# Optimization experiments

Measured on AMD Instinct MI355X. Metric: run time of the kernel, lower is better.

## Reference

```python
import jax, jax.numpy as jnp
import numpy as np

H, D = 16, 64            # heads_num, mouse_hidden_dim // heads_num
START_FRAME = 9728       # current_start (token units)
GLOBAL_END_PREV = 9728   # kv_cache['global_end_index'] before this call
LOCAL_END_PREV = 9728    # kv_cache['local_end_index'] before this call
SINK = 0                 # sink_tokens in source
WINDOW = 8192            # max_attention_size = local_attn_size (token units)


def _rope_interleaved(x, cos_h, sin_h):
    # non-neox (interleaved) rotary: x [B,S,H,D], cos_h/sin_h [S, D//2]
    x1 = x[..., 0::2]
    x2 = x[..., 1::2]
    c = cos_h[None, :, None, :]
    s = sin_h[None, :, None, :]
    o1 = x1 * c - x2 * s
    o2 = x2 * c + x1 * s
    return jnp.stack([o1, o2], axis=-1).reshape(x.shape)


def setup_inputs() -> dict:
    key = jax.random.key(0)
    ks = jax.random.split(key, 7)
    B, S, C = 1, 1024, 10240
    return {
        'q': jax.random.normal(ks[0], (B, S, H, D), jnp.float32),
        'k': jax.random.normal(ks[1], (B, S, H, D), jnp.float32),
        'v': jax.random.normal(ks[2], (B, S, H, D), jnp.float32),
        'cache_k': jax.random.normal(ks[3], (B, C, H, D), jnp.float32),
        'cache_v': jax.random.normal(ks[4], (B, C, H, D), jnp.float32),
        'freqs_cos': jax.random.uniform(ks[5], (START_FRAME + S, D), jnp.float32, -1.0, 1.0),
        'freqs_sin': jax.random.uniform(ks[6], (START_FRAME + S, D), jnp.float32, -1.0, 1.0),
    }


def reference(q, k, v, cache_k, cache_v, freqs_cos, freqs_sin):
    B, S, _, _ = q.shape
    # _apply_rotary_emb_qk: slice freqs at start_offset, take every-other col (cos_half)
    cos_h = freqs_cos[START_FRAME:START_FRAME + S, ::2]  # [S, D//2]
    sin_h = freqs_sin[START_FRAME:START_FRAME + S, ::2]
    q_r = _rope_interleaved(q, cos_h, sin_h)
    k_r = _rope_interleaved(k, cos_h, sin_h)

    # ring-buffer KV-cache update (all index math is static Python ints)
    current_end = START_FRAME + S
    cache_size = cache_k.shape[1]
    num_new = S
    if current_end > GLOBAL_END_PREV and num_new + LOCAL_END_PREV > cache_size:
        num_evicted = num_new + LOCAL_END_PREV - cache_size
        num_rolled = LOCAL_END_PREV - num_evicted - SINK
        rolled_k = jax.lax.dynamic_slice_in_dim(cache_k, SINK + num_evicted, num_rolled, axis=1)
        rolled_v = jax.lax.dynamic_slice_in_dim(cache_v, SINK + num_evicted, num_rolled, axis=1)
        cache_k = cache_k.at[:, SINK:SINK + num_rolled].set(rolled_k)
        cache_v = cache_v.at[:, SINK:SINK + num_rolled].set(rolled_v)
        local_end = LOCAL_END_PREV + current_end - GLOBAL_END_PREV - num_evicted
    else:
        local_end = LOCAL_END_PREV + current_end - GLOBAL_END_PREV
    local_start = local_end - num_new
    cache_k = cache_k.at[:, local_start:local_end].set(k_r)
    cache_v = cache_v.at[:, local_start:local_end].set(v)

    # windowed (last local_attn_size tokens) non-causal attention
    cache_start = max(0, local_end - WINDOW)
    wk = cache_k[:, cache_start:local_end]  # [B, W, H, D]
    wv = cache_v[:, cache_start:local_end]
    scale = 1.0 / np.float32(np.sqrt(D))
    scores = jnp.einsum('bqhd,bkhd->bhqk', q_r, wk) * scale
    probs = jax.nn.softmax(scores, axis=-1)
    out = jnp.einsum('bhqk,bkhd->bqhd', probs, wv)
    return out.reshape(B, S, H * D)
```

## Files before the change

kernel.cpp:

```cpp
#include <hip/hip_runtime.h>

#define HH 16
#define DD 64
#define SQ 1024
#define LW 8192
#define OLDK 7168
#define CACHE_BASE 2560
#define SFRAME 9728
#define KSPLIT 8
#define KPER (LW / KSPLIT)
#define NSTEP (KPER / 64)

#define KB_OFF 0u
#define VT_OFF 16777216u
#define QB_OFF 33554432u
#define OP_OFF 35651584u
#define LP_OFF 69206016u

typedef __bf16 bf16x8 __attribute__((ext_vector_type(8)));
typedef float floatx16 __attribute__((ext_vector_type(16)));
typedef float floatx2 __attribute__((ext_vector_type(2)));
typedef unsigned uintx2 __attribute__((ext_vector_type(2)));
typedef unsigned uintx4 __attribute__((ext_vector_type(4)));

__device__ __forceinline__ unsigned short f2bf(float f) {
  unsigned u = __builtin_bit_cast(unsigned, f);
  u += 0x7fffu + ((u >> 16) & 1u);
  return (unsigned short)(u >> 16);
}

__device__ __forceinline__ float fast_exp2(float x) {
#if __has_builtin(__builtin_amdgcn_exp2f)
  return __builtin_amdgcn_exp2f(x);
#else
  return __builtin_exp2f(x);
#endif
}

__device__ __forceinline__ unsigned pack_bf2(float a, float b) {
#if __has_builtin(__builtin_amdgcn_cvt_pk_bf16_f32)
  typedef __bf16 bf16x2_t __attribute__((ext_vector_type(2)));
  bf16x2_t r = __builtin_amdgcn_cvt_pk_bf16_f32(a, b);
  return __builtin_bit_cast(unsigned, r);
#else
  unsigned ua = __builtin_bit_cast(unsigned, a) + 0x8000u;
  unsigned ub = __builtin_bit_cast(unsigned, b) + 0x8000u;
  return __builtin_amdgcn_perm(ub, ua, 0x07060302);
#endif
}

__device__ __forceinline__ void async16(void* lds, const void* g) {
  __builtin_amdgcn_global_load_lds((__attribute__((address_space(1))) void*)(g),
                                   (__attribute__((address_space(3))) void*)(lds),
                                   16, 0, 0);
}

__global__ __launch_bounds__(256) void prepass(
    const float* __restrict__ qin, const float* __restrict__ kin,
    const float* __restrict__ vin, const float* __restrict__ ck,
    const float* __restrict__ cv, const float* __restrict__ fc,
    const float* __restrict__ fs, unsigned short* __restrict__ Kb,
    unsigned short* __restrict__ Vt, unsigned short* __restrict__ Qb) {
  int b = blockIdx.x, t = threadIdx.x;
  if (b < 1024) {
    __shared__ float tl[128 * 65];
    int h = b >> 6, kk0 = (b & 63) * 128;
    int c = t & 15;
#pragma unroll
    for (int it = 0; it < 8; it++) {
      int kk = it * 16 + (t >> 4);
      int gk = kk0 + kk;
      const float* src = (gk < OLDK)
                             ? cv + (CACHE_BASE + gk) * (HH * DD) + h * DD + 4 * c
                             : vin + (gk - OLDK) * (HH * DD) + h * DD + 4 * c;
      float4 vv = *(const float4*)src;
      *(float4*)(tl + kk * 65 + c * 4) = vv;
    }
    __syncthreads();
    int kq = t & 15;
#pragma unroll
    for (int jt = 0; jt < 4; jt++) {
      int d = jt * 16 + (t >> 4);
      ushort4 lo, hi;
      unsigned short tmp[8];
#pragma unroll
      for (int j = 0; j < 8; j++) {
        int kk = 8 * kq + j;
        tmp[j] = f2bf(tl[kk * 65 + d]);
      }
      lo.x = tmp[0]; lo.y = tmp[1]; lo.z = tmp[2]; lo.w = tmp[3];
      hi.x = tmp[4]; hi.y = tmp[5]; hi.z = tmp[6]; hi.w = tmp[7];
      unsigned short* dst = Vt + (h * DD + d) * LW + kk0 + 8 * kq;
      *(ushort4*)(dst) = lo;
      *(ushort4*)(dst + 4) = hi;
    }
  } else if (b < 8192) {
    int b1 = b - 1024;
    int h = b1 / 448, g = b1 % 448;
    int kk = g * 16 + (t >> 4);
    int lane = t & 15;
    float4 val = *(const float4*)(ck + (CACHE_BASE + kk) * (HH * DD) + h * DD + lane * 4);
    ushort4 o;
    o.x = f2bf(val.x); o.y = f2bf(val.y); o.z = f2bf(val.z); o.w = f2bf(val.w);
    *(ushort4*)(Kb + (h * LW + kk) * DD + lane * 4) = o;
  } else if (b < 10240) {
    int b2 = b - 8192;
    int rh = b2 * 8 + (t >> 5);
    int s = rh >> 4, h = rh & 15, i = t & 31;
    float2 x = *(const float2*)(kin + s * (HH * DD) + h * DD + 2 * i);
    float c = fc[(SFRAME + s) * DD + 2 * i];
    float sn = fs[(SFRAME + s) * DD + 2 * i];
    ushort2 o;
    o.x = f2bf(x.x * c - x.y * sn);
    o.y = f2bf(x.y * c + x.x * sn);
    *(ushort2*)(Kb + (h * LW + OLDK + s) * DD + 2 * i) = o;
  } else {
    int b3 = b - 10240;
    int rh = b3 * 8 + (t >> 5);
    int s = rh >> 4, h = rh & 15, i = t & 31;
    const float SC = 0.18033688011112042f;
    float2 x = *(const float2*)(qin + s * (HH * DD) + h * DD + 2 * i);
    float c = fc[(SFRAME + s) * DD + 2 * i];
    float sn = fs[(SFRAME + s) * DD + 2 * i];
    ushort2 o;
    o.x = f2bf((x.x * c - x.y * sn) * SC);
    o.y = f2bf((x.y * c + x.x * sn) * SC);
    *(ushort2*)(Qb + (h * SQ + s) * DD + 2 * i) = o;
  }
}

__global__ __launch_bounds__(256, 2) void attn(
    const unsigned short* __restrict__ Kb, const unsigned short* __restrict__ Vt,
    const unsigned short* __restrict__ Qb, unsigned short* __restrict__ Op,
    float* __restrict__ Lp) {
  __shared__ __align__(16) unsigned char sK[2][8192];
  __shared__ __align__(16) unsigned char sV[2][8192];

  int bid = blockIdx.x;
  int g = bid & 127, qb = bid >> 7;
  int h = g & 15, ks = g >> 4;
  int t = threadIdx.x;
  int w = t >> 6, lane = t & 63;
  int l31 = lane & 31, e = lane >> 5;
  int q0 = qb * 256 + w * 64;

  int baseA = (l31 & 7) ^ ((l31 >> 3) & 7);
  int baseB = (l31 & 7) ^ (((l31 >> 3) + 4) & 7);

  bf16x8 qf[2][4];
#pragma unroll
  for (int tq = 0; tq < 2; tq++) {
    const unsigned short* qptr = Qb + (h * SQ + q0 + 32 * tq + l31) * DD + 8 * e;
#pragma unroll
    for (int c = 0; c < 4; c++) qf[tq][c] = *(const bf16x8*)(qptr + 16 * c);
  }

  floatx16 o[2][2];
#pragma unroll
  for (int a = 0; a < 2; a++)
#pragma unroll
    for (int bb = 0; bb < 2; bb++)
#pragma unroll
      for (int i = 0; i < 16; i++) o[a][bb][i] = 0.f;
  float ls[2] = {0.f, 0.f};

  const floatx16 fz = {0.f};

  const unsigned short* KbH = Kb + h * (LW * DD);
  const unsigned short* VtH = Vt + h * (DD * LW);
  int kkBase = ks * KPER;

  auto stage = [&](int buf, int kk0) {
#pragma unroll
    for (int hf = 0; hf < 2; hf++) {
      int gi = w * 128 + hf * 64 + lane;
      int rr = gi >> 3;
      int src = (gi & 7) ^ (rr & 7) ^ ((rr >> 3) & 7);
      async16(sK[buf] + gi * 16, KbH + (kk0 + rr) * DD + src * 8);
      async16(sV[buf] + gi * 16, VtH + rr * LW + kk0 + src * 8);
    }
  };

  auto softmax_half = [&](floatx16& sv, int tq, int tk, bf16x8 pf[2][4]) {
#pragma unroll
    for (int i = 0; i < 16; i++) sv[i] = fast_exp2(sv[i]);
    floatx2 t0, t1, t2, t3;
    t0[0] = sv[0];  t0[1] = sv[1];
    t1[0] = sv[2];  t1[1] = sv[3];
    t2[0] = sv[4];  t2[1] = sv[5];
    t3[0] = sv[6];  t3[1] = sv[7];
    floatx2 u0 = t0 + t1, u1 = t2 + t3;
    floatx2 t4, t5, t6, t7;
    t4[0] = sv[8];  t4[1] = sv[9];
    t5[0] = sv[10]; t5[1] = sv[11];
    t6[0] = sv[12]; t6[1] = sv[13];
    t7[0] = sv[14]; t7[1] = sv[15];
    floatx2 u2 = t4 + t5, u3 = t6 + t7;
    floatx2 v0 = u0 + u1, v1 = u2 + u3;
    floatx2 vs = v0 + v1;
    ls[tq] += vs[0] + vs[1];
#pragma unroll
    for (int kcp = 0; kcp < 2; kcp++) {
      unsigned u0p = pack_bf2(sv[8 * kcp + 0], sv[8 * kcp + 1]);
      unsigned u1p = pack_bf2(sv[8 * kcp + 2], sv[8 * kcp + 3]);
      unsigned u2p = pack_bf2(sv[8 * kcp + 4], sv[8 * kcp + 5]);
      unsigned u3p = pack_bf2(sv[8 * kcp + 6], sv[8 * kcp + 7]);
      uintx2 r0 = __builtin_amdgcn_permlane32_swap(u0p, u2p, false, false);
      uintx2 r1 = __builtin_amdgcn_permlane32_swap(u1p, u3p, false, false);
      uintx4 f;
      f[0] = r0[0]; f[1] = r1[0]; f[2] = r0[1]; f[3] = r1[1];
      pf[tq][2 * tk + kcp] = __builtin_bit_cast(bf16x8, f);
    }
  };

  stage(0, kkBase);

  for (int st = 0; st < NSTEP; st++) {
    __syncthreads();
    const unsigned char* cK = sK[st & 1];
    const unsigned char* cV = sV[st & 1];

    bf16x8 pf[2][4];

    floatx16 sA0, sA1;
    {
      int p0 = e ^ baseA;
      bf16x8 ka0 = *(const bf16x8*)(cK + (l31 * 8 + p0) * 16);
      sA0 = __builtin_amdgcn_mfma_f32_32x32x16_bf16(ka0, qf[0][0], fz, 0, 0, 0);
      sA1 = __builtin_amdgcn_mfma_f32_32x32x16_bf16(ka0, qf[1][0], fz, 0, 0, 0);
#pragma unroll
      for (int c = 1; c < 4; c++) {
        int p = (2 * c + e) ^ baseA;
        bf16x8 ka = *(const bf16x8*)(cK + (l31 * 8 + p) * 16);
        sA0 = __builtin_amdgcn_mfma_f32_32x32x16_bf16(ka, qf[0][c], sA0, 0, 0, 0);
        sA1 = __builtin_amdgcn_mfma_f32_32x32x16_bf16(ka, qf[1][c], sA1, 0, 0, 0);
      }
    }

    if (st + 1 < NSTEP) stage((st + 1) & 1, kkBase + (st + 1) * 64);

    floatx16 sB0, sB1;
    {
      int p0 = e ^ baseB;
      bf16x8 kb0 = *(const bf16x8*)(cK + ((l31 + 32) * 8 + p0) * 16);
      sB0 = __builtin_amdgcn_mfma_f32_32x32x16_bf16(kb0, qf[0][0], fz, 0, 0, 0);
      sB1 = __builtin_amdgcn_mfma_f32_32x32x16_bf16(kb0, qf[1][0], fz, 0, 0, 0);
#pragma unroll
      for (int c = 1; c < 4; c++) {
        int p = (2 * c + e) ^ baseB;
        bf16x8 kb = *(const bf16x8*)(cK + ((l31 + 32) * 8 + p) * 16);
        sB0 = __builtin_amdgcn_mfma_f32_32x32x16_bf16(kb, qf[0][c], sB0, 0, 0, 0);
        sB1 = __builtin_amdgcn_mfma_f32_32x32x16_bf16(kb, qf[1][c], sB1, 0, 0, 0);
      }
    }

    softmax_half(sA0, 0, 0, pf);
    softmax_half(sA1, 1, 0, pf);

#pragma unroll
    for (int kc = 0; kc < 2; kc++) {
      int pA = (2 * kc + e) ^ baseA;
      int pB = (2 * kc + e) ^ baseB;
      bf16x8 va = *(const bf16x8*)(cV + (l31 * 8 + pA) * 16);
      bf16x8 vb = *(const bf16x8*)(cV + ((l31 + 32) * 8 + pB) * 16);
      o[0][0] = __builtin_amdgcn_mfma_f32_32x32x16_bf16(va, pf[0][kc], o[0][0], 0, 0, 0);
      o[0][1] = __builtin_amdgcn_mfma_f32_32x32x16_bf16(vb, pf[0][kc], o[0][1], 0, 0, 0);
      o[1][0] = __builtin_amdgcn_mfma_f32_32x32x16_bf16(va, pf[1][kc], o[1][0], 0, 0, 0);
      o[1][1] = __builtin_amdgcn_mfma_f32_32x32x16_bf16(vb, pf[1][kc], o[1][1], 0, 0, 0);
    }

    softmax_half(sB0, 0, 1, pf);
    softmax_half(sB1, 1, 1, pf);

#pragma unroll
    for (int kc = 2; kc < 4; kc++) {
      int pA = (2 * kc + e) ^ baseA;
      int pB = (2 * kc + e) ^ baseB;
      bf16x8 va = *(const bf16x8*)(cV + (l31 * 8 + pA) * 16);
      bf16x8 vb = *(const bf16x8*)(cV + ((l31 + 32) * 8 + pB) * 16);
      o[0][0] = __builtin_amdgcn_mfma_f32_32x32x16_bf16(va, pf[0][kc], o[0][0], 0, 0, 0);
      o[0][1] = __builtin_amdgcn_mfma_f32_32x32x16_bf16(vb, pf[0][kc], o[0][1], 0, 0, 0);
      o[1][0] = __builtin_amdgcn_mfma_f32_32x32x16_bf16(va, pf[1][kc], o[1][0], 0, 0, 0);
      o[1][1] = __builtin_amdgcn_mfma_f32_32x32x16_bf16(vb, pf[1][kc], o[1][1], 0, 0, 0);
    }
  }

#pragma unroll
  for (int tq = 0; tq < 2; tq++) {
    float l = ls[tq];
    l += __shfl_xor(l, 32, 64);
    int qrow = q0 + 32 * tq + l31;
    unsigned short* op = Op + (((ks * 16 + h) * SQ) + qrow) * DD;
#pragma unroll
    for (int t4 = 0; t4 < 4; t4++) {
      uint2 a, b;
      a.x = pack_bf2(o[tq][0][4 * t4 + 0], o[tq][0][4 * t4 + 1]);
      a.y = pack_bf2(o[tq][0][4 * t4 + 2], o[tq][0][4 * t4 + 3]);
      b.x = pack_bf2(o[tq][1][4 * t4 + 0], o[tq][1][4 * t4 + 1]);
      b.y = pack_bf2(o[tq][1][4 * t4 + 2], o[tq][1][4 * t4 + 3]);
      *(uint2*)(op + 8 * t4 + 4 * e) = a;
      *(uint2*)(op + 32 + 8 * t4 + 4 * e) = b;
    }
    if (e == 0) Lp[(ks * 16 + h) * SQ + qrow] = l;
  }
}

__global__ __launch_bounds__(256) void combine(const unsigned short* __restrict__ Op,
                                               const float* __restrict__ Lp,
                                               float* __restrict__ out) {
  int idx = blockIdx.x * 256 + threadIdx.x;
  int d4 = idx & 15, q = (idx >> 4) & 1023, h = idx >> 14;
  float num[4] = {0.f, 0.f, 0.f, 0.f};
  float den = 0.f;
#pragma unroll
  for (int s = 0; s < KSPLIT; s++) {
    int row = (s * 16 + h) * SQ + q;
    uint2 pkv = *(const uint2*)(Op + row * DD + 4 * d4);
    num[0] += __builtin_bit_cast(float, pkv.x << 16);
    num[1] += __builtin_bit_cast(float, pkv.x & 0xffff0000u);
    num[2] += __builtin_bit_cast(float, pkv.y << 16);
    num[3] += __builtin_bit_cast(float, pkv.y & 0xffff0000u);
    den += Lp[row];
  }
  float r = 1.0f / den;
  float4 ov;
  ov.x = num[0] * r; ov.y = num[1] * r; ov.z = num[2] * r; ov.w = num[3] * r;
  *(float4*)(out + q * (HH * DD) + h * DD + 4 * d4) = ov;
}

extern "C" void kernel_launch(void* const* d_in, const int* in_sizes, int n_in,
                              void* d_out, int out_size, void* d_ws, size_t ws_size,
                              hipStream_t stream) {
  const float* q  = (const float*)d_in[0];
  const float* k  = (const float*)d_in[1];
  const float* v  = (const float*)d_in[2];
  const float* ck = (const float*)d_in[3];
  const float* cv = (const float*)d_in[4];
  const float* fc = (const float*)d_in[5];
  const float* fs = (const float*)d_in[6];
  float* out = (float*)d_out;
  char* ws = (char*)d_ws;

  unsigned short* Kb = (unsigned short*)(ws + KB_OFF);
  unsigned short* Vt = (unsigned short*)(ws + VT_OFF);
  unsigned short* Qb = (unsigned short*)(ws + QB_OFF);
  unsigned short* Op = (unsigned short*)(ws + OP_OFF);
  float* Lp = (float*)(ws + LP_OFF);

  prepass<<<12288, 256, 0, stream>>>(q, k, v, ck, cv, fc, fs, Kb, Vt, Qb);
  attn<<<512, 256, 0, stream>>>(Kb, Vt, Qb, Op, Lp);
  combine<<<1024, 256, 0, stream>>>(Op, Lp, out);
}
```

Baseline: 176.7 us.

## Halve per-wave query tile, double attn grid, raise occupancy, add MFMA priority hints

Each wave now handles 32 query rows instead of 64, so the attention grid doubles to 1024 blocks and the launch bound asks for 4 blocks per CU instead of 2. The aim is lower register pressure, higher occupancy and more latency hiding. s_setprio hints are placed around the MFMA sections so waves in matrix phases get scheduling priority. The cost is that each K/V tile staged in shared memory is reused by half as many query rows, which doubles K/V global and LDS traffic per query.

New measurement: 178.4 us. About the same (+1.0%).

```diff
diff --git a/kernel.cpp b/kernel.cpp
--- a/kernel.cpp
+++ b/kernel.cpp
@@ -129,7 +129,7 @@
   }
 }
 
-__global__ __launch_bounds__(256, 2) void attn(
+__global__ __launch_bounds__(256, 4) void attn(
     const unsigned short* __restrict__ Kb, const unsigned short* __restrict__ Vt,
     const unsigned short* __restrict__ Qb, unsigned short* __restrict__ Op,
     float* __restrict__ Lp) {
@@ -142,27 +142,24 @@
   int t = threadIdx.x;
   int w = t >> 6, lane = t & 63;
   int l31 = lane & 31, e = lane >> 5;
-  int q0 = qb * 256 + w * 64;
+  int q0 = qb * 128 + w * 32;
 
   int baseA = (l31 & 7) ^ ((l31 >> 3) & 7);
   int baseB = (l31 & 7) ^ (((l31 >> 3) + 4) & 7);
 
-  bf16x8 qf[2][4];
-#pragma unroll
-  for (int tq = 0; tq < 2; tq++) {
-    const unsigned short* qptr = Qb + (h * SQ + q0 + 32 * tq + l31) * DD + 8 * e;
-#pragma unroll
-    for (int c = 0; c < 4; c++) qf[tq][c] = *(const bf16x8*)(qptr + 16 * c);
-  }
-
-  floatx16 o[2][2];
-#pragma unroll
-  for (int a = 0; a < 2; a++)
-#pragma unroll
-    for (int bb = 0; bb < 2; bb++)
-#pragma unroll
-      for (int i = 0; i < 16; i++) o[a][bb][i] = 0.f;
-  float ls[2] = {0.f, 0.f};
+  bf16x8 qf[4];
+  {
+    const unsigned short* qptr = Qb + (h * SQ + q0 + l31) * DD + 8 * e;
+#pragma unroll
+    for (int c = 0; c < 4; c++) qf[c] = *(const bf16x8*)(qptr + 16 * c);
+  }
+
+  floatx16 o[2];
+#pragma unroll
+  for (int bb = 0; bb < 2; bb++)
+#pragma unroll
+    for (int i = 0; i < 16; i++) o[bb][i] = 0.f;
+  float ls = 0.f;
 
   const floatx16 fz = {0.f};
 
@@ -181,7 +178,7 @@
     }
   };
 
-  auto softmax_half = [&](floatx16& sv, int tq, int tk, bf16x8 pf[2][4]) {
+  auto softmax_half = [&](floatx16& sv, int tk, bf16x8* pf) {
 #pragma unroll
     for (int i = 0; i < 16; i++) sv[i] = fast_exp2(sv[i]);
     floatx2 t0, t1, t2, t3;
@@ -198,7 +195,7 @@
     floatx2 u2 = t4 + t5, u3 = t6 + t7;
     floatx2 v0 = u0 + u1, v1 = u2 + u3;
     floatx2 vs = v0 + v1;
-    ls[tq] += vs[0] + vs[1];
+    ls += vs[0] + vs[1];
 #pragma unroll
     for (int kcp = 0; kcp < 2; kcp++) {
       unsigned u0p = pack_bf2(sv[8 * kcp + 0], sv[8 * kcp + 1]);
@@ -209,7 +206,7 @@
       uintx2 r1 = __builtin_amdgcn_permlane32_swap(u1p, u3p, false, false);
       uintx4 f;
       f[0] = r0[0]; f[1] = r1[0]; f[2] = r0[1]; f[3] = r1[1];
-      pf[tq][2 * tk + kcp] = __builtin_bit_cast(bf16x8, f);
+      pf[2 * tk + kcp] = __builtin_bit_cast(bf16x8, f);
     }
   };
 
@@ -220,84 +217,81 @@
     const unsigned char* cK = sK[st & 1];
     const unsigned char* cV = sV[st & 1];
 
-    bf16x8 pf[2][4];
-
-    floatx16 sA0, sA1;
+    bf16x8 pf[4];
+
+    floatx16 sA;
+    __builtin_amdgcn_s_setprio(1);
     {
       int p0 = e ^ baseA;
       bf16x8 ka0 = *(const bf16x8*)(cK + (l31 * 8 + p0) * 16);
-      sA0 = __builtin_amdgcn_mfma_f32_32x32x16_bf16(ka0, qf[0][0], fz, 0, 0, 0);
-      sA1 = __builtin_amdgcn_mfma_f32_32x32x16_bf16(ka0, qf[1][0], fz, 0, 0, 0);
+      sA = __builtin_amdgcn_mfma_f32_32x32x16_bf16(ka0, qf[0], fz, 0, 0, 0);
 #pragma unroll
       for (int c = 1; c < 4; c++) {
         int p = (2 * c + e) ^ baseA;
         bf16x8 ka = *(const bf16x8*)(cK + (l31 * 8 + p) * 16);
-        sA0 = __builtin_amdgcn_mfma_f32_32x32x16_bf16(ka, qf[0][c], sA0, 0, 0, 0);
-        sA1 = __builtin_amdgcn_mfma_f32_32x32x16_bf16(ka, qf[1][c], sA1, 0, 0, 0);
+        sA = __builtin_amdgcn_mfma_f32_32x32x16_bf16(ka, qf[c], sA, 0, 0, 0);
       }
     }
+    __builtin_amdgcn_s_setprio(0);
 
     if (st + 1 < NSTEP) stage((st + 1) & 1, kkBase + (st + 1) * 64);
 
-    floatx16 sB0, sB1;
+    floatx16 sB;
+    __builtin_amdgcn_s_setprio(1);
     {
       int p0 = e ^ baseB;
       bf16x8 kb0 = *(const bf16x8*)(cK + ((l31 + 32) * 8 + p0) * 16);
-      sB0 = __builtin_amdgcn_mfma_f32_32x32x16_bf16(kb0, qf[0][0], fz, 0, 0, 0);
-      sB1 = __builtin_amdgcn_mfma_f32_32x32x16_bf16(kb0, qf[1][0], fz, 0, 0, 0);
+      sB = __builtin_amdgcn_mfma_f32_32x32x16_bf16(kb0, qf[0], fz, 0, 0, 0);
 #pragma unroll
       for (int c = 1; c < 4; c++) {
         int p = (2 * c + e) ^ baseB;
         bf16x8 kb = *(const bf16x8*)(cK + ((l31 + 32) * 8 + p) * 16);
-        sB0 = __builtin_amdgcn_mfma_f32_32x32x16_bf16(kb, qf[0][c], sB0, 0, 0, 0);
-        sB1 = __builtin_amdgcn_mfma_f32_32x32x16_bf16(kb, qf[1][c], sB1, 0, 0, 0);
+        sB = __builtin_amdgcn_mfma_f32_32x32x16_bf16(kb, qf[c], sB, 0, 0, 0);
       }
     }
-
-    softmax_half(sA0, 0, 0, pf);
-    softmax_half(sA1, 1, 0, pf);
-
+    __builtin_amdgcn_s_setprio(0);
+
+    softmax_half(sA, 0, pf);
+
+    __builtin_amdgcn_s_setprio(1);
 #pragma unroll
     for (int kc = 0; kc < 2; kc++) {
       int pA = (2 * kc + e) ^ baseA;
       int pB = (2 * kc + e) ^ baseB;
       bf16x8 va = *(const bf16x8*)(cV + (l31 * 8 + pA) * 16);
       bf16x8 vb = *(const bf16x8*)(cV + ((l31 + 32) * 8 + pB) * 16);
-      o[0][0] = __builtin_amdgcn_mfma_f32_32x32x16_bf16(va, pf[0][kc], o[0][0], 0, 0, 0);
-      o[0][1] = __builtin_amdgcn_mfma_f32_32x32x16_bf16(vb, pf[0][kc], o[0][1], 0, 0, 0);
-      o[1][0] = __builtin_amdgcn_mfma_f32_32x32x16_bf16(va, pf[1][kc], o[1][0], 0, 0, 0);
-      o[1][1] = __builtin_amdgcn_mfma_f32_32x32x16_bf16(vb, pf[1][kc], o[1][1], 0, 0, 0);
-    }
-
-    softmax_half(sB0, 0, 1, pf);
-    softmax_half(sB1, 1, 1, pf);
-
+      o[0] = __builtin_amdgcn_mfma_f32_32x32x16_bf16(va, pf[kc], o[0], 0, 0, 0);
+      o[1] = __builtin_amdgcn_mfma_f32_32x32x16_bf16(vb, pf[kc], o[1], 0, 0, 0);
+    }
+    __builtin_amdgcn_s_setprio(0);
+
+    softmax_half(sB, 1, pf);
+
+    __builtin_amdgcn_s_setprio(1);
 #pragma unroll
     for (int kc = 2; kc < 4; kc++) {
       int pA = (2 * kc + e) ^ baseA;
       int pB = (2 * kc + e) ^ baseB;
       bf16x8 va = *(const bf16x8*)(cV + (l31 * 8 + pA) * 16);
       bf16x8 vb = *(const bf16x8*)(cV + ((l31 + 32) * 8 + pB) * 16);
-      o[0][0] = __builtin_amdgcn_mfma_f32_32x32x16_bf16(va, pf[0][kc], o[0][0], 0, 0, 0);
-      o[0][1] = __builtin_amdgcn_mfma_f32_32x32x16_bf16(vb, pf[0][kc], o[0][1], 0, 0, 0);
-      o[1][0] = __builtin_amdgcn_mfma_f32_32x32x16_bf16(va, pf[1][kc], o[1][0], 0, 0, 0);
-      o[1][1] = __builtin_amdgcn_mfma_f32_32x32x16_bf16(vb, pf[1][kc], o[1][1], 0, 0, 0);
-    }
-  }
-
-#pragma unroll
-  for (int tq = 0; tq < 2; tq++) {
-    float l = ls[tq];
+      o[0] = __builtin_amdgcn_mfma_f32_32x32x16_bf16(va, pf[kc], o[0], 0, 0, 0);
+      o[1] = __builtin_amdgcn_mfma_f32_32x32x16_bf16(vb, pf[kc], o[1], 0, 0, 0);
+    }
+    __builtin_amdgcn_s_setprio(0);
+  }
+
+  {
+    float l = ls;
     l += __shfl_xor(l, 32, 64);
-    int qrow = q0 + 32 * tq + l31;
+    int qrow = q0 + l31;
     unsigned short* op = Op + (((ks * 16 + h) * SQ) + qrow) * DD;
 #pragma unroll
     for (int t4 = 0; t4 < 4; t4++) {
       uint2 a, b;
-      a.x = pack_bf2(o[tq][0][4 * t4 + 0], o[tq][0][4 * t4 + 1]);
-      a.y = pack_bf2(o[tq][0][4 * t4 + 2], o[tq][0][4 * t4 + 3]);
-      b.x = pack_bf2(o[tq][1][4 * t4 + 0], o[tq][1][4 * t4 + 1]);
-      b.y = pack_bf2(o[tq][1][4 * t4 + 2], o[tq][1][4 * t4 + 3]);
+      a.x = pack_bf2(o[0][4 * t4 + 0], o[0][4 * t4 + 1]);
+      a.y = pack_bf2(o[0][4 * t4 + 2], o[0][4 * t4 + 3]);
+      b.x = pack_bf2(o[1][4 * t4 + 0], o[1][4 * t4 + 1]);
+      b.y = pack_bf2(o[1][4 * t4 + 2], o[1][4 * t4 + 3]);
       *(uint2*)(op + 8 * t4 + 4 * e) = a;
       *(uint2*)(op + 32 + 8 * t4 + 4 * e) = b;
     }
@@ -348,6 +342,6 @@
   float* Lp = (float*)(ws + LP_OFF);
 
   prepass<<<12288, 256, 0, stream>>>(q, k, v, ck, cv, fc, fs, Kb, Vt, Qb);
-  attn<<<512, 256, 0, stream>>>(Kb, Vt, Qb, Op, Lp);
+  attn<<<1024, 256, 0, stream>>>(Kb, Vt, Qb, Op, Lp);
   combine<<<1024, 256, 0, stream>>>(Op, Lp, out);
 }
```
